# Kernel optimization log

Measured on AMD Instinct MI355X. Metric: run time of the kernel, lower is better.

## Reference

```python
import jax, jax.numpy as jnp
import numpy as np

B, S, H, E, K = 4, 4096, 4096, 64, 2
AUX_W = 0.01


def setup_inputs() -> dict:
    key = jax.random.key(0)
    k1, k2 = jax.random.split(key)
    hidden_states = jax.random.normal(k1, (B, S, H), dtype=jnp.float32)
    W = jax.random.normal(k2, (E, H), dtype=jnp.float32) * 0.02  # router weight [num_experts, hidden_size]
    return {"hidden_states": hidden_states, "W": W}


def reference(hidden_states, W):
    b, s, h = hidden_states.shape
    n = b * s  # tokens
    e, k = W.shape[0], K
    # router logits: [b, s, e] -> [n, e]
    logits = jnp.einsum('bsh,eh->bse', hidden_states, W).reshape(n, e)
    probs = jax.nn.softmax(logits, axis=-1)
    # top-k routing
    routing_weights, selected_experts = jax.lax.top_k(probs, k)  # [n, k]
    routing_weights = routing_weights / jnp.sum(routing_weights, axis=-1, keepdims=True)
    # scatter_add normalized weights back onto expert axis: [n, e]
    rows = jnp.arange(n)[:, None]
    router_prob_per_expert = jnp.zeros((n, e), dtype=probs.dtype).at[rows, selected_experts].add(routing_weights)
    aux_loss = jnp.mean(jnp.sum(router_prob_per_expert, axis=0) * jnp.mean(router_prob_per_expert, axis=0)) * e * AUX_W
    # expert mask via one-hot: [n, k, e]
    dispatch_mask = jax.nn.one_hot(selected_experts, e, dtype=hidden_states.dtype)
    combine_weights = routing_weights.reshape(b, s, k, 1)
    return (dispatch_mask, combine_weights, aux_loss)
```

## Files before the change

### kernel.cpp

```cpp
#include <hip/hip_runtime.h>
#include <hip/hip_bf16.h>
#include <cstdint>

#define N_TOK 16384
#define HID   4096
#define NEXP  64
#define AUXW  0.01f

typedef const __attribute__((address_space(1))) void gvoid_t;
typedef __attribute__((address_space(3))) void lvoid_t;

__device__ __forceinline__ void async_cp16(const void* gsrc, void* ldst) {
  __builtin_amdgcn_global_load_lds((gvoid_t*)gsrc, (lvoid_t*)ldst, 16, 0, 0);
}

__global__ __launch_bounds__(512, 2) void router_main(
    const float* __restrict__ hs, const float* __restrict__ Wg,
    float* __restrict__ out, float* __restrict__ Sacc) {
  __shared__ char smem[65536];
  float* lds = (float*)smem;

  const int tid  = threadIdx.x;
  const int kg   = tid >> 8;
  const int t256 = tid & 255;
  const int tx   = t256 & 15;
  const int ty   = t256 >> 4;
  const int tb   = blockIdx.x << 6;

  float acc[4][4];
#pragma unroll
  for (int i = 0; i < 4; ++i)
#pragma unroll
    for (int j = 0; j < 4; ++j) acc[i][j] = 0.f;

  auto stage = [&](int buf, int chunk) {
    const int k0 = chunk << 6;
    float* dst = lds + buf * 8192;
#pragma unroll
    for (int it = 0; it < 2; ++it) {
      int G = tid + (it << 9);
      int row = G >> 4, g = G & 15;
      int gs = g ^ (row & 15);
      async_cp16(hs + (size_t)(tb + row) * HID + k0 + (gs << 2), dst + (G << 2));
    }
#pragma unroll
    for (int it = 0; it < 2; ++it) {
      int G = tid + (it << 9);
      int row = G >> 4, g = G & 15;
      int gs = g ^ (row & 15);
      async_cp16(Wg + (size_t)row * HID + k0 + (gs << 2), dst + 4096 + (G << 2));
    }
  };

  auto compute = [&](int buf) {
    const float* hsb = lds + buf * 8192;
    const float* Wb  = hsb + 4096;
    const int kb = kg << 5;
#pragma unroll
    for (int kk = 0; kk < 32; kk += 4) {
      const int kq = (kb + kk) >> 2;
      float4 a[4], b[4];
#pragma unroll
      for (int i = 0; i < 4; ++i) {
        int row = ty + (i << 4);
        a[i] = *(const float4*)(hsb + (row << 6) + ((kq ^ ty) << 2));
      }
#pragma unroll
      for (int j = 0; j < 4; ++j) {
        int row = tx + (j << 4);
        b[j] = *(const float4*)(Wb + (row << 6) + ((kq ^ tx) << 2));
      }
#pragma unroll
      for (int i = 0; i < 4; ++i)
#pragma unroll
        for (int j = 0; j < 4; ++j) {
          acc[i][j] = fmaf(a[i].x, b[j].x, acc[i][j]);
          acc[i][j] = fmaf(a[i].y, b[j].y, acc[i][j]);
          acc[i][j] = fmaf(a[i].z, b[j].z, acc[i][j]);
          acc[i][j] = fmaf(a[i].w, b[j].w, acc[i][j]);
        }
    }
  };

  stage(0, 0);
  __syncthreads();
  for (int c = 0; c < 63; ++c) {
    stage((c + 1) & 1, c + 1);
    compute(c & 1);
    __syncthreads();
  }
  compute(1);
  __syncthreads();

  float* red   = lds;
  float* lg    = lds + 4096;
  float* S_lds = lds + 4096 + 64 * 73;
  int*   e1a   = (int*)(S_lds + 64);
  int*   e2a   = e1a + 64;

  if (kg == 1) {
#pragma unroll
    for (int i = 0; i < 4; ++i)
#pragma unroll
      for (int j = 0; j < 4; ++j) red[t256 * 16 + i * 4 + j] = acc[i][j];
  }
  if (tid < 64) S_lds[tid] = 0.f;
  __syncthreads();

  if (kg == 0) {
#pragma unroll
    for (int i = 0; i < 4; ++i)
#pragma unroll
      for (int j = 0; j < 4; ++j) {
        float v = acc[i][j] + red[t256 * 16 + i * 4 + j];
        lg[(ty + (i << 4)) * 73 + tx + (j << 4)] = v;
      }
  }
  __syncthreads();

  if (tid < 64) {
    const float* row = lg + tid * 73;
    float m1 = -1e30f, m2 = -1e30f;
    int   i1 = 0,      i2 = 0;
    for (int e = 0; e < NEXP; ++e) {
      float v = row[e];
      if (v > m1)      { m2 = m1; i2 = i1; m1 = v; i1 = e; }
      else if (v > m2) { m2 = v;  i2 = e; }
    }
    float q  = expf(m2 - m1);
    float w1 = 1.f / (1.f + q);
    float w2 = q * w1;
    float* comb = out + (size_t)N_TOK * 2 * NEXP;
    comb[(size_t)(tb + tid) * 2]     = w1;
    comb[(size_t)(tb + tid) * 2 + 1] = w2;
    e1a[tid] = i1;
    e2a[tid] = i2;
    atomicAdd(&S_lds[i1], w1);
    atomicAdd(&S_lds[i2], w2);
  }
  __syncthreads();

  if (tid < 64) atomicAdd(&Sacc[tid], S_lds[tid]);

#pragma unroll
  for (int it = 0; it < 4; ++it) {
    int f   = it * 512 + tid;
    int tok = f >> 5;
    int rem = f & 31;
    int sl  = rem >> 4;
    int g   = rem & 15;
    int sel = sl ? e2a[tok] : e1a[tok];
    float4 v; v.x = v.y = v.z = v.w = 0.f;
    int base = g << 2;
    if (sel >= base && sel < base + 4) ((float*)&v)[sel - base] = 1.0f;
    *(float4*)(out + ((size_t)(tb + tok) * 2 + sl) * 64 + base) = v;
  }
}

__global__ void aux_k(const float* __restrict__ S, float* __restrict__ out) {
  float v = S[threadIdx.x];
  float s = v * v;
#pragma unroll
  for (int off = 32; off > 0; off >>= 1) s += __shfl_down(s, off);
  if (threadIdx.x == 0)
    out[(size_t)N_TOK * 2 * NEXP + (size_t)N_TOK * 2] = s * (AUXW / (float)N_TOK);
}

extern "C" void kernel_launch(void* const* d_in, const int* in_sizes, int n_in,
                              void* d_out, int out_size, void* d_ws, size_t ws_size,
                              hipStream_t stream) {
  const float* hs = (const float*)d_in[0];
  const float* Wg = (const float*)d_in[1];
  float* out = (float*)d_out;
  float* S   = (float*)d_ws;
  hipMemsetAsync(d_ws, 0, NEXP * sizeof(float), stream);
  hipLaunchKernelGGL(router_main, dim3(N_TOK / 64), dim3(512), 0, stream,
                     hs, Wg, out, S);
  hipLaunchKernelGGL(aux_k, dim3(1), dim3(64), 0, stream, S, out);
}
```

Measured before the change: 463.4 us.

## Use fp16 MFMA with three-way split emulating fp32 router GEMM

Replaces the scalar FP32 FMA GEMM with fp16 16x16x32 MFMA instructions. Each fp32 operand is split into three fp16 parts (high, mid, low), and six cross products are accumulated to approximate fp32 accuracy. The tile shrinks to 32 tokens per 256-thread block, with register-staged global loads replacing the async LDS copies. This moves the compute onto matrix cores but adds conversion work per element. The fp16 split may lose precision on values outside fp16 range and could change top-k ties.

```diff
diff --git a/kernel.cpp b/kernel.cpp
--- a/kernel.cpp
+++ b/kernel.cpp
@@ -6,153 +6,185 @@
 #define HID   4096
 #define NEXP  64
 #define AUXW  0.01f
-
-typedef const __attribute__((address_space(1))) void gvoid_t;
-typedef __attribute__((address_space(3))) void lvoid_t;
-
-__device__ __forceinline__ void async_cp16(const void* gsrc, void* ldst) {
-  __builtin_amdgcn_global_load_lds((gvoid_t*)gsrc, (lvoid_t*)ldst, 16, 0, 0);
-}
-
-__global__ __launch_bounds__(512, 2) void router_main(
+#define TOKB  32
+#define KC    32
+#define NCH   (HID/KC)
+
+typedef __attribute__((ext_vector_type(4))) _Float16 f16x4;
+typedef __attribute__((ext_vector_type(8))) _Float16 f16x8;
+typedef __attribute__((ext_vector_type(4))) float f32x4;
+
+#define AH 0
+#define AM 2048
+#define AL 4096
+#define WH 6144
+#define WM 10240
+#define WL 14336
+#define BUFSZ 18432
+
+__device__ __forceinline__ void split3(float4 p, f16x4& H, f16x4& M, f16x4& L) {
+  float f[4] = {p.x, p.y, p.z, p.w};
+  f16x4 h, m, l;
+#pragma unroll
+  for (int j = 0; j < 4; ++j) {
+    _Float16 hh = (_Float16)f[j];
+    float r1 = f[j] - (float)hh;
+    _Float16 mm = (_Float16)r1;
+    float r2 = r1 - (float)mm;
+    h[j] = hh; m[j] = mm; l[j] = (_Float16)r2;
+  }
+  H = h; M = m; L = l;
+}
+
+__global__ __launch_bounds__(256, 2) void router_main(
     const float* __restrict__ hs, const float* __restrict__ Wg,
     float* __restrict__ out, float* __restrict__ Sacc) {
-  __shared__ char smem[65536];
-  float* lds = (float*)smem;
+  __shared__ __align__(16) char smem[2 * BUFSZ];
 
   const int tid  = threadIdx.x;
-  const int kg   = tid >> 8;
-  const int t256 = tid & 255;
-  const int tx   = t256 & 15;
-  const int ty   = t256 >> 4;
-  const int tb   = blockIdx.x << 6;
-
-  float acc[4][4];
-#pragma unroll
-  for (int i = 0; i < 4; ++i)
-#pragma unroll
-    for (int j = 0; j < 4; ++j) acc[i][j] = 0.f;
-
-  auto stage = [&](int buf, int chunk) {
-    const int k0 = chunk << 6;
-    float* dst = lds + buf * 8192;
-#pragma unroll
-    for (int it = 0; it < 2; ++it) {
-      int G = tid + (it << 9);
-      int row = G >> 4, g = G & 15;
-      int gs = g ^ (row & 15);
-      async_cp16(hs + (size_t)(tb + row) * HID + k0 + (gs << 2), dst + (G << 2));
+  const int tb   = blockIdx.x * TOKB;
+  const int lane = tid & 63;
+  const int wv   = tid >> 6;
+  const int l15  = lane & 15;
+  const int l4   = lane >> 4;
+  const int rbase = (wv >> 1) * 16;
+  const int cbase = (wv & 1) * 32;
+
+  const int sa_row = tid >> 3, sa_fq = tid & 7;
+  const int q1 = tid + 256;
+  const int sw_row1 = q1 >> 3, sw_fq1 = q1 & 7;
+
+  f32x4 acc0 = {0.f, 0.f, 0.f, 0.f}, acc1 = {0.f, 0.f, 0.f, 0.f};
+
+  char* b0 = smem;
+  char* b1 = smem + BUFSZ;
+
+  const int a_r = rbase + l15;
+  const int aoff = a_r * 64 + ((l4 ^ (a_r & 3)) << 4);
+  const int e0r = cbase + l15;
+  const int e1r = cbase + 16 + l15;
+  const int boff0 = e0r * 64 + ((l4 ^ (e0r & 3)) << 4);
+  const int boff1 = e1r * 64 + ((l4 ^ (e1r & 3)) << 4);
+
+  auto compute = [&](const char* buf) {
+    f16x8 ah = *(const f16x8*)(buf + AH + aoff);
+    f16x8 am = *(const f16x8*)(buf + AM + aoff);
+    f16x8 al = *(const f16x8*)(buf + AL + aoff);
+    f16x8 bh0 = *(const f16x8*)(buf + WH + boff0);
+    f16x8 bm0 = *(const f16x8*)(buf + WM + boff0);
+    f16x8 bl0 = *(const f16x8*)(buf + WL + boff0);
+    f16x8 bh1 = *(const f16x8*)(buf + WH + boff1);
+    f16x8 bm1 = *(const f16x8*)(buf + WM + boff1);
+    f16x8 bl1 = *(const f16x8*)(buf + WL + boff1);
+    acc0 = __builtin_amdgcn_mfma_f32_16x16x32_f16(ah, bh0, acc0, 0, 0, 0);
+    acc1 = __builtin_amdgcn_mfma_f32_16x16x32_f16(ah, bh1, acc1, 0, 0, 0);
+    acc0 = __builtin_amdgcn_mfma_f32_16x16x32_f16(ah, bm0, acc0, 0, 0, 0);
+    acc1 = __builtin_amdgcn_mfma_f32_16x16x32_f16(ah, bm1, acc1, 0, 0, 0);
+    acc0 = __builtin_amdgcn_mfma_f32_16x16x32_f16(am, bh0, acc0, 0, 0, 0);
+    acc1 = __builtin_amdgcn_mfma_f32_16x16x32_f16(am, bh1, acc1, 0, 0, 0);
+    acc0 = __builtin_amdgcn_mfma_f32_16x16x32_f16(ah, bl0, acc0, 0, 0, 0);
+    acc1 = __builtin_amdgcn_mfma_f32_16x16x32_f16(ah, bl1, acc1, 0, 0, 0);
+    acc0 = __builtin_amdgcn_mfma_f32_16x16x32_f16(al, bh0, acc0, 0, 0, 0);
+    acc1 = __builtin_amdgcn_mfma_f32_16x16x32_f16(al, bh1, acc1, 0, 0, 0);
+    acc0 = __builtin_amdgcn_mfma_f32_16x16x32_f16(am, bm0, acc0, 0, 0, 0);
+    acc1 = __builtin_amdgcn_mfma_f32_16x16x32_f16(am, bm1, acc1, 0, 0, 0);
+  };
+
+  auto stage_write = [&](char* buf, float4 A0, float4 W0, float4 W1) {
+    f16x4 H, M, L;
+    split3(A0, H, M, L);
+    int off = sa_row * 64 + (((sa_fq >> 1) ^ (sa_row & 3)) << 4) + (sa_fq & 1) * 8;
+    *(f16x4*)(buf + AH + off) = H;
+    *(f16x4*)(buf + AM + off) = M;
+    *(f16x4*)(buf + AL + off) = L;
+    split3(W0, H, M, L);
+    off = sa_row * 64 + (((sa_fq >> 1) ^ (sa_row & 3)) << 4) + (sa_fq & 1) * 8;
+    *(f16x4*)(buf + WH + off) = H;
+    *(f16x4*)(buf + WM + off) = M;
+    *(f16x4*)(buf + WL + off) = L;
+    split3(W1, H, M, L);
+    off = sw_row1 * 64 + (((sw_fq1 >> 1) ^ (sw_row1 & 3)) << 4) + (sw_fq1 & 1) * 8;
+    *(f16x4*)(buf + WH + off) = H;
+    *(f16x4*)(buf + WM + off) = M;
+    *(f16x4*)(buf + WL + off) = L;
+  };
+
+  auto load3 = [&](int c, float4& A0, float4& W0, float4& W1) {
+    A0 = *(const float4*)(hs + (size_t)(tb + sa_row) * HID + c * KC + sa_fq * 4);
+    W0 = *(const float4*)(Wg + (size_t)sa_row * HID + c * KC + sa_fq * 4);
+    W1 = *(const float4*)(Wg + (size_t)sw_row1 * HID + c * KC + sw_fq1 * 4);
+  };
+
+  {
+    float4 A0, W0, W1;
+    load3(0, A0, W0, W1);
+    stage_write(b0, A0, W0, W1);
+  }
+  __syncthreads();
+
+#pragma unroll 2
+  for (int c = 0; c < NCH - 1; ++c) {
+    float4 A0, W0, W1;
+    load3(c + 1, A0, W0, W1);
+    compute((c & 1) ? b1 : b0);
+    stage_write(((c + 1) & 1) ? b1 : b0, A0, W0, W1);
+    __syncthreads();
+  }
+  compute(b1);
+
+  float* lg    = (float*)smem;
+  float* S_lds = lg + TOKB * 73;
+  int*   e1a   = (int*)(S_lds + 64);
+  int*   e2a   = e1a + 32;
+
+  {
+    const int orow = rbase + l4 * 4;
+    const int ocol = cbase + l15;
+#pragma unroll
+    for (int r = 0; r < 4; ++r) {
+      lg[(orow + r) * 73 + ocol]      = acc0[r];
+      lg[(orow + r) * 73 + ocol + 16] = acc1[r];
     }
-#pragma unroll
-    for (int it = 0; it < 2; ++it) {
-      int G = tid + (it << 9);
-      int row = G >> 4, g = G & 15;
-      int gs = g ^ (row & 15);
-      async_cp16(Wg + (size_t)row * HID + k0 + (gs << 2), dst + 4096 + (G << 2));
-    }
-  };
-
-  auto compute = [&](int buf) {
-    const float* hsb = lds + buf * 8192;
-    const float* Wb  = hsb + 4096;
-    const int kb = kg << 5;
-#pragma unroll
-    for (int kk = 0; kk < 32; kk += 4) {
-      const int kq = (kb + kk) >> 2;
-      float4 a[4], b[4];
-#pragma unroll
-      for (int i = 0; i < 4; ++i) {
-        int row = ty + (i << 4);
-        a[i] = *(const float4*)(hsb + (row << 6) + ((kq ^ ty) << 2));
-      }
-#pragma unroll
-      for (int j = 0; j < 4; ++j) {
-        int row = tx + (j << 4);
-        b[j] = *(const float4*)(Wb + (row << 6) + ((kq ^ tx) << 2));
-      }
-#pragma unroll
-      for (int i = 0; i < 4; ++i)
-#pragma unroll
-        for (int j = 0; j < 4; ++j) {
-          acc[i][j] = fmaf(a[i].x, b[j].x, acc[i][j]);
-          acc[i][j] = fmaf(a[i].y, b[j].y, acc[i][j]);
-          acc[i][j] = fmaf(a[i].z, b[j].z, acc[i][j]);
-          acc[i][j] = fmaf(a[i].w, b[j].w, acc[i][j]);
-        }
-    }
-  };
-
-  stage(0, 0);
-  __syncthreads();
-  for (int c = 0; c < 63; ++c) {
-    stage((c + 1) & 1, c + 1);
-    compute(c & 1);
-    __syncthreads();
-  }
-  compute(1);
-  __syncthreads();
-
-  float* red   = lds;
-  float* lg    = lds + 4096;
-  float* S_lds = lds + 4096 + 64 * 73;
-  int*   e1a   = (int*)(S_lds + 64);
-  int*   e2a   = e1a + 64;
-
-  if (kg == 1) {
-#pragma unroll
-    for (int i = 0; i < 4; ++i)
-#pragma unroll
-      for (int j = 0; j < 4; ++j) red[t256 * 16 + i * 4 + j] = acc[i][j];
   }
   if (tid < 64) S_lds[tid] = 0.f;
   __syncthreads();
 
-  if (kg == 0) {
-#pragma unroll
-    for (int i = 0; i < 4; ++i)
-#pragma unroll
-      for (int j = 0; j < 4; ++j) {
-        float v = acc[i][j] + red[t256 * 16 + i * 4 + j];
-        lg[(ty + (i << 4)) * 73 + tx + (j << 4)] = v;
-      }
-  }
-  __syncthreads();
-
-  if (tid < 64) {
+  if (tid < TOKB) {
     const float* row = lg + tid * 73;
     float m1 = -1e30f, m2 = -1e30f;
-    int   i1 = 0,      i2 = 0;
+    int i1 = 0, i2 = 0;
     for (int e = 0; e < NEXP; ++e) {
       float v = row[e];
       if (v > m1)      { m2 = m1; i2 = i1; m1 = v; i1 = e; }
       else if (v > m2) { m2 = v;  i2 = e; }
     }
-    float q  = expf(m2 - m1);
-    float w1 = 1.f / (1.f + q);
-    float w2 = q * w1;
+    float qq = expf(m2 - m1);
+    float w1 = 1.f / (1.f + qq);
+    float w2 = qq * w1;
     float* comb = out + (size_t)N_TOK * 2 * NEXP;
     comb[(size_t)(tb + tid) * 2]     = w1;
     comb[(size_t)(tb + tid) * 2 + 1] = w2;
-    e1a[tid] = i1;
-    e2a[tid] = i2;
+    e1a[tid] = i1; e2a[tid] = i2;
     atomicAdd(&S_lds[i1], w1);
     atomicAdd(&S_lds[i2], w2);
   }
   __syncthreads();
-
-  if (tid < 64) atomicAdd(&Sacc[tid], S_lds[tid]);
+  if (tid < 64) {
+    float s = S_lds[tid];
+    if (s != 0.f) atomicAdd(&Sacc[tid], s);
+  }
 
 #pragma unroll
   for (int it = 0; it < 4; ++it) {
-    int f   = it * 512 + tid;
-    int tok = f >> 5;
-    int rem = f & 31;
-    int sl  = rem >> 4;
-    int g   = rem & 15;
+    int f = it * 256 + tid;
+    int tok = f >> 5, rem = f & 31, sl = rem >> 4, g = rem & 15;
     int sel = sl ? e2a[tok] : e1a[tok];
-    float4 v; v.x = v.y = v.z = v.w = 0.f;
     int base = g << 2;
-    if (sel >= base && sel < base + 4) ((float*)&v)[sel - base] = 1.0f;
+    float4 v;
+    v.x = (sel == base)     ? 1.f : 0.f;
+    v.y = (sel == base + 1) ? 1.f : 0.f;
+    v.z = (sel == base + 2) ? 1.f : 0.f;
+    v.w = (sel == base + 3) ? 1.f : 0.f;
     *(float4*)(out + ((size_t)(tb + tok) * 2 + sl) * 64 + base) = v;
   }
 }
@@ -174,7 +206,7 @@
   float* out = (float*)d_out;
   float* S   = (float*)d_ws;
   hipMemsetAsync(d_ws, 0, NEXP * sizeof(float), stream);
-  hipLaunchKernelGGL(router_main, dim3(N_TOK / 64), dim3(512), 0, stream,
+  hipLaunchKernelGGL(router_main, dim3(N_TOK / TOKB), dim3(256), 0, stream,
                      hs, Wg, out, S);
   hipLaunchKernelGGL(aux_k, dim3(1), dim3(64), 0, stream, S, out);
 }
```

Result: faster. 425.1 us (-8.3%).

## Use fp16 triple-split MFMA for router GEMM with presplit weight image

Applied to the files above, without the earlier changes.

Replaces the fp32 FMA-based router GEMM with fp16 MFMA instructions. Both operands are split into high, mid and low fp16 parts, and six cross products are accumulated to keep near-fp32 accuracy. A new prepass kernel writes the weight matrix as a swizzled fp16 split image into the workspace. Hidden states are loaded into registers and split on the fly. The block tile shrinks to 32 tokens on 256 threads with double-buffered weight staging. This targets the FMA-bound compute of the fp32 GEMM, at the cost of an extra launch, split-conversion ALU work and a small accuracy risk from the split approximation.

```diff
diff --git a/kernel.cpp b/kernel.cpp
--- a/kernel.cpp
+++ b/kernel.cpp
@@ -1,158 +1,228 @@
 #include <hip/hip_runtime.h>
-#include <hip/hip_bf16.h>
 #include <cstdint>
 
 #define N_TOK 16384
 #define HID   4096
 #define NEXP  64
 #define AUXW  0.01f
+#define TOKB  32
+#define KC    64
+#define NCH   (HID/KC)
+#define IMG_CHUNK 24576
+
+typedef __attribute__((ext_vector_type(4))) _Float16 f16x4;
+typedef __attribute__((ext_vector_type(8))) _Float16 f16x8;
+typedef __attribute__((ext_vector_type(4))) float f32x4;
 
 typedef const __attribute__((address_space(1))) void gvoid_t;
 typedef __attribute__((address_space(3))) void lvoid_t;
 
-__device__ __forceinline__ void async_cp16(const void* gsrc, void* ldst) {
-  __builtin_amdgcn_global_load_lds((gvoid_t*)gsrc, (lvoid_t*)ldst, 16, 0, 0);
-}
-
-__global__ __launch_bounds__(512, 2) void router_main(
-    const float* __restrict__ hs, const float* __restrict__ Wg,
+__device__ __forceinline__ void async_cp16(const void* g, void* l) {
+  __builtin_amdgcn_global_load_lds((gvoid_t*)g, (lvoid_t*)l, 16, 0, 0);
+}
+
+__device__ __forceinline__ void split3_f4(float4 p, f16x4& H, f16x4& M, f16x4& L) {
+  float f[4] = {p.x, p.y, p.z, p.w};
+#pragma unroll
+  for (int j = 0; j < 4; ++j) {
+    _Float16 h = (_Float16)f[j];
+    float r1 = f[j] - (float)h;
+    _Float16 m = (_Float16)r1;
+    float r2 = r1 - (float)m;
+    H[j] = h; M[j] = m; L[j] = (_Float16)r2;
+  }
+}
+
+__global__ void presplit_w(const float* __restrict__ Wg, char* __restrict__ img) {
+  int id = blockIdx.x * 256 + threadIdx.x;
+  int row = id >> 9;
+  int rem = id & 511;
+  int chunk = rem >> 3;
+  int g = rem & 7;
+  const float* src = Wg + (size_t)row * HID + chunk * KC + g * 8;
+  float4 p0 = *(const float4*)src;
+  float4 p1 = *(const float4*)(src + 4);
+  f16x4 h0, m0, l0, h1, m1, l1;
+  split3_f4(p0, h0, m0, l0);
+  split3_f4(p1, h1, m1, l1);
+  char* base = img + (size_t)chunk * IMG_CHUNK + row * 128 + ((g ^ (row & 7)) << 4);
+  *(f16x4*)(base)         = h0;  *(f16x4*)(base + 8)     = h1;
+  *(f16x4*)(base + 8192)  = m0;  *(f16x4*)(base + 8200)  = m1;
+  *(f16x4*)(base + 16384) = l0;  *(f16x4*)(base + 16392) = l1;
+}
+
+__global__ __launch_bounds__(256, 2) void router_main(
+    const float* __restrict__ hs, const char* __restrict__ wimg,
     float* __restrict__ out, float* __restrict__ Sacc) {
-  __shared__ char smem[65536];
-  float* lds = (float*)smem;
-
-  const int tid  = threadIdx.x;
-  const int kg   = tid >> 8;
-  const int t256 = tid & 255;
-  const int tx   = t256 & 15;
-  const int ty   = t256 >> 4;
-  const int tb   = blockIdx.x << 6;
-
-  float acc[4][4];
-#pragma unroll
-  for (int i = 0; i < 4; ++i)
-#pragma unroll
-    for (int j = 0; j < 4; ++j) acc[i][j] = 0.f;
-
-  auto stage = [&](int buf, int chunk) {
-    const int k0 = chunk << 6;
-    float* dst = lds + buf * 8192;
-#pragma unroll
-    for (int it = 0; it < 2; ++it) {
-      int G = tid + (it << 9);
-      int row = G >> 4, g = G & 15;
-      int gs = g ^ (row & 15);
-      async_cp16(hs + (size_t)(tb + row) * HID + k0 + (gs << 2), dst + (G << 2));
-    }
-#pragma unroll
-    for (int it = 0; it < 2; ++it) {
-      int G = tid + (it << 9);
-      int row = G >> 4, g = G & 15;
-      int gs = g ^ (row & 15);
-      async_cp16(Wg + (size_t)row * HID + k0 + (gs << 2), dst + 4096 + (G << 2));
-    }
-  };
-
-  auto compute = [&](int buf) {
-    const float* hsb = lds + buf * 8192;
-    const float* Wb  = hsb + 4096;
-    const int kb = kg << 5;
-#pragma unroll
-    for (int kk = 0; kk < 32; kk += 4) {
-      const int kq = (kb + kk) >> 2;
-      float4 a[4], b[4];
-#pragma unroll
-      for (int i = 0; i < 4; ++i) {
-        int row = ty + (i << 4);
-        a[i] = *(const float4*)(hsb + (row << 6) + ((kq ^ ty) << 2));
+  __shared__ __align__(16) char smem[61440];
+  char* Abuf = smem;
+  char* Wb0 = smem + 12288;
+  char* Wb1 = smem + 36864;
+
+  const int tid = threadIdx.x;
+  const int tb = blockIdx.x * TOKB;
+  const int lane = tid & 63;
+  const int wv = tid >> 6;
+  const int eg = wv & 1, kg = wv >> 1;
+  const int l15 = lane & 15, l4 = lane >> 4;
+
+  const int srow = tid >> 3, sg = tid & 7;
+  const float* hsp = hs + (size_t)(tb + srow) * HID + sg * 8;
+  const int aslot = srow * 128 + ((sg ^ (srow & 7)) << 4);
+  const char* wsrc = wimg + tid * 16;
+
+  int aoff[2], boff[2];
+#pragma unroll
+  for (int tg = 0; tg < 2; ++tg) {
+    int r = tg * 16 + l15;
+    aoff[tg] = r * 128 + (((kg * 4 + l4) ^ (r & 7)) << 4);
+  }
+#pragma unroll
+  for (int bg = 0; bg < 2; ++bg) {
+    int r = eg * 32 + bg * 16 + l15;
+    boff[bg] = r * 128 + (((kg * 4 + l4) ^ (r & 7)) << 4);
+  }
+
+  f32x4 acc[2][2] = {};
+  float4 rA0, rA1, rB0, rB1;
+
+  auto loadhs = [&](int c, float4& x0, float4& x1) {
+    x0 = *(const float4*)(hsp + (size_t)c * KC);
+    x1 = *(const float4*)(hsp + (size_t)c * KC + 4);
+  };
+  auto stageW = [&](int c, char* dst) {
+#pragma unroll
+    for (int it = 0; it < 6; ++it)
+      async_cp16(wsrc + (size_t)c * IMG_CHUNK + it * 4096, dst + it * 4096 + tid * 16);
+  };
+  auto writeA = [&](float4 x0, float4 x1) {
+    f16x4 h0, m0, l0, h1, m1, l1;
+    split3_f4(x0, h0, m0, l0);
+    split3_f4(x1, h1, m1, l1);
+    f16x8 H, M, L;
+#pragma unroll
+    for (int j = 0; j < 4; ++j) {
+      H[j] = h0[j]; H[j + 4] = h1[j];
+      M[j] = m0[j]; M[j + 4] = m1[j];
+      L[j] = l0[j]; L[j + 4] = l1[j];
+    }
+    *(f16x8*)(Abuf + aslot)        = H;
+    *(f16x8*)(Abuf + 4096 + aslot) = M;
+    *(f16x8*)(Abuf + 8192 + aslot) = L;
+  };
+  auto compute = [&](const char* W) {
+    f16x8 aH[2], aM[2], aL[2], bH[2], bM[2], bL[2];
+#pragma unroll
+    for (int t = 0; t < 2; ++t) {
+      aH[t] = *(const f16x8*)(Abuf + aoff[t]);
+      aM[t] = *(const f16x8*)(Abuf + 4096 + aoff[t]);
+      aL[t] = *(const f16x8*)(Abuf + 8192 + aoff[t]);
+    }
+#pragma unroll
+    for (int b = 0; b < 2; ++b) {
+      bH[b] = *(const f16x8*)(W + boff[b]);
+      bM[b] = *(const f16x8*)(W + 8192 + boff[b]);
+      bL[b] = *(const f16x8*)(W + 16384 + boff[b]);
+    }
+#pragma unroll
+    for (int t = 0; t < 2; ++t)
+#pragma unroll
+      for (int b = 0; b < 2; ++b) {
+        f32x4 a = acc[t][b];
+        a = __builtin_amdgcn_mfma_f32_16x16x32_f16(aH[t], bH[b], a, 0, 0, 0);
+        a = __builtin_amdgcn_mfma_f32_16x16x32_f16(aH[t], bM[b], a, 0, 0, 0);
+        a = __builtin_amdgcn_mfma_f32_16x16x32_f16(aM[t], bH[b], a, 0, 0, 0);
+        a = __builtin_amdgcn_mfma_f32_16x16x32_f16(aH[t], bL[b], a, 0, 0, 0);
+        a = __builtin_amdgcn_mfma_f32_16x16x32_f16(aL[t], bH[b], a, 0, 0, 0);
+        a = __builtin_amdgcn_mfma_f32_16x16x32_f16(aM[t], bM[b], a, 0, 0, 0);
+        acc[t][b] = a;
       }
-#pragma unroll
-      for (int j = 0; j < 4; ++j) {
-        int row = tx + (j << 4);
-        b[j] = *(const float4*)(Wb + (row << 6) + ((kq ^ tx) << 2));
-      }
-#pragma unroll
-      for (int i = 0; i < 4; ++i)
-#pragma unroll
-        for (int j = 0; j < 4; ++j) {
-          acc[i][j] = fmaf(a[i].x, b[j].x, acc[i][j]);
-          acc[i][j] = fmaf(a[i].y, b[j].y, acc[i][j]);
-          acc[i][j] = fmaf(a[i].z, b[j].z, acc[i][j]);
-          acc[i][j] = fmaf(a[i].w, b[j].w, acc[i][j]);
+  };
+
+  loadhs(0, rA0, rA1);
+  stageW(0, Wb0);
+  writeA(rA0, rA1);
+  loadhs(1, rA0, rA1);
+  __syncthreads();
+
+  for (int c = 0; c < NCH - 1; ++c) {
+    stageW(c + 1, (c & 1) ? Wb0 : Wb1);
+    int cn = (c + 2 < NCH) ? c + 2 : NCH - 1;
+    loadhs(cn, rB0, rB1);
+    compute((c & 1) ? Wb1 : Wb0);
+    asm volatile("s_waitcnt lgkmcnt(0)\n\ts_barrier" ::: "memory");
+    writeA(rA0, rA1);
+    rA0 = rB0; rA1 = rB1;
+    __syncthreads();
+  }
+  compute((NCH - 1) & 1 ? Wb1 : Wb0);
+
+  float* red   = (float*)(smem + 12288);
+  float* lg    = (float*)(smem + 20480);
+  float* S_lds = (float*)(smem + 29824);
+  int*   e1a   = (int*)(smem + 30080);
+  int*   e2a   = (int*)(smem + 30208);
+
+  if (kg == 1) {
+#pragma unroll
+    for (int t = 0; t < 2; ++t)
+#pragma unroll
+      for (int b = 0; b < 2; ++b)
+#pragma unroll
+        for (int r = 0; r < 4; ++r)
+          red[(t * 16 + l4 * 4 + r) * 64 + eg * 32 + b * 16 + l15] = acc[t][b][r];
+  }
+  if (tid < 64) S_lds[tid] = 0.f;
+  __syncthreads();
+  if (kg == 0) {
+#pragma unroll
+    for (int t = 0; t < 2; ++t)
+#pragma unroll
+      for (int b = 0; b < 2; ++b)
+#pragma unroll
+        for (int r = 0; r < 4; ++r) {
+          int tok = t * 16 + l4 * 4 + r, ex = eg * 32 + b * 16 + l15;
+          lg[tok * 73 + ex] = acc[t][b][r] + red[tok * 64 + ex];
         }
-    }
-  };
-
-  stage(0, 0);
-  __syncthreads();
-  for (int c = 0; c < 63; ++c) {
-    stage((c + 1) & 1, c + 1);
-    compute(c & 1);
-    __syncthreads();
-  }
-  compute(1);
-  __syncthreads();
-
-  float* red   = lds;
-  float* lg    = lds + 4096;
-  float* S_lds = lds + 4096 + 64 * 73;
-  int*   e1a   = (int*)(S_lds + 64);
-  int*   e2a   = e1a + 64;
-
-  if (kg == 1) {
-#pragma unroll
-    for (int i = 0; i < 4; ++i)
-#pragma unroll
-      for (int j = 0; j < 4; ++j) red[t256 * 16 + i * 4 + j] = acc[i][j];
-  }
-  if (tid < 64) S_lds[tid] = 0.f;
-  __syncthreads();
-
-  if (kg == 0) {
-#pragma unroll
-    for (int i = 0; i < 4; ++i)
-#pragma unroll
-      for (int j = 0; j < 4; ++j) {
-        float v = acc[i][j] + red[t256 * 16 + i * 4 + j];
-        lg[(ty + (i << 4)) * 73 + tx + (j << 4)] = v;
-      }
-  }
-  __syncthreads();
-
-  if (tid < 64) {
+  }
+  __syncthreads();
+
+  if (tid < TOKB) {
     const float* row = lg + tid * 73;
     float m1 = -1e30f, m2 = -1e30f;
-    int   i1 = 0,      i2 = 0;
+    int i1 = 0, i2 = 0;
     for (int e = 0; e < NEXP; ++e) {
       float v = row[e];
       if (v > m1)      { m2 = m1; i2 = i1; m1 = v; i1 = e; }
       else if (v > m2) { m2 = v;  i2 = e; }
     }
-    float q  = expf(m2 - m1);
-    float w1 = 1.f / (1.f + q);
-    float w2 = q * w1;
+    float qq = expf(m2 - m1);
+    float w1 = 1.f / (1.f + qq);
+    float w2 = qq * w1;
     float* comb = out + (size_t)N_TOK * 2 * NEXP;
     comb[(size_t)(tb + tid) * 2]     = w1;
     comb[(size_t)(tb + tid) * 2 + 1] = w2;
-    e1a[tid] = i1;
-    e2a[tid] = i2;
+    e1a[tid] = i1; e2a[tid] = i2;
     atomicAdd(&S_lds[i1], w1);
     atomicAdd(&S_lds[i2], w2);
   }
   __syncthreads();
-
-  if (tid < 64) atomicAdd(&Sacc[tid], S_lds[tid]);
+  if (tid < 64) {
+    float s = S_lds[tid];
+    if (s != 0.f) atomicAdd(&Sacc[tid], s);
+  }
 
 #pragma unroll
   for (int it = 0; it < 4; ++it) {
-    int f   = it * 512 + tid;
-    int tok = f >> 5;
-    int rem = f & 31;
-    int sl  = rem >> 4;
-    int g   = rem & 15;
+    int f = it * 256 + tid;
+    int tok = f >> 5, rem = f & 31, sl = rem >> 4, g = rem & 15;
     int sel = sl ? e2a[tok] : e1a[tok];
-    float4 v; v.x = v.y = v.z = v.w = 0.f;
     int base = g << 2;
-    if (sel >= base && sel < base + 4) ((float*)&v)[sel - base] = 1.0f;
+    float4 v;
+    v.x = (sel == base)     ? 1.f : 0.f;
+    v.y = (sel == base + 1) ? 1.f : 0.f;
+    v.z = (sel == base + 2) ? 1.f : 0.f;
+    v.w = (sel == base + 3) ? 1.f : 0.f;
     *(float4*)(out + ((size_t)(tb + tok) * 2 + sl) * 64 + base) = v;
   }
 }
@@ -172,9 +242,11 @@
   const float* hs = (const float*)d_in[0];
   const float* Wg = (const float*)d_in[1];
   float* out = (float*)d_out;
-  float* S   = (float*)d_ws;
-  hipMemsetAsync(d_ws, 0, NEXP * sizeof(float), stream);
-  hipLaunchKernelGGL(router_main, dim3(N_TOK / 64), dim3(512), 0, stream,
-                     hs, Wg, out, S);
+  float* S = (float*)d_ws;
+  char* img = (char*)d_ws + 256;
+  hipMemsetAsync(d_ws, 0, 256, stream);
+  hipLaunchKernelGGL(presplit_w, dim3(128), dim3(256), 0, stream, Wg, img);
+  hipLaunchKernelGGL(router_main, dim3(N_TOK / TOKB), dim3(256), 0, stream,
+                     hs, img, out, S);
   hipLaunchKernelGGL(aux_k, dim3(1), dim3(64), 0, stream, S, out);
 }
```

New measurement: 391.2 us. 1.18x faster.
